# Kernel tuning notes

Hardware: AMD Instinct MI355X
Metric: run time of the kernel (lower is better)

Reference implementation:

```python
import jax, jax.numpy as jnp
import numpy as np

N_NODES = 50000
N_EDGES = 800000
SD = 128
N_GRAPHS = 128
HL = 4
VOCAB = 1340
N_CLASSES = 41
BN_EPS = 1e-5


def setup_inputs() -> dict:
    key = jax.random.key(0)
    ks = jax.random.split(key, 20)
    s = 1.0 / np.sqrt(SD)
    inp = {
        "node_ids": jax.random.randint(ks[0], (N_NODES,), 0, VOCAB),
        "edge_index": jax.random.randint(ks[1], (2, N_EDGES), 0, N_NODES),
        "batch": jnp.sort(jax.random.randint(ks[2], (N_NODES,), 0, N_GRAPHS)),
        "emb": jax.random.normal(ks[3], (VOCAB, SD)) * 0.05,
        "in_W1": jax.random.normal(ks[4], (SD, SD)) * s,
        "in_b1": jnp.zeros((SD,)),
        "in_W2": jax.random.normal(ks[5], (SD, SD)) * s,
        "in_b2": jnp.zeros((SD,)),
        "bn_gamma": jnp.ones((SD,)),
        "bn_beta": jnp.zeros((SD,)),
        "bn_mean": jnp.zeros((SD,)),
        "bn_var": jnp.ones((SD,)),
        "out_W1": jax.random.normal(ks[6], (SD, SD)) * s,
        "out_b1": jnp.zeros((SD,)),
        "out_W2": jax.random.normal(ks[7], (SD, SD)) * s,
        "out_b2": jnp.zeros((SD,)),
        "fc1_W": jax.random.normal(ks[8], (SD, SD)) * s,
        "fc1_b": jnp.zeros((SD,)),
        "fc2_W": jax.random.normal(ks[9], (N_CLASSES, SD)) * s,
        "fc2_b": jnp.zeros((N_CLASSES,)),
    }
    return inp


def reference(node_ids, edge_index, batch, emb, in_W1, in_b1, in_W2, in_b2,
              bn_gamma, bn_beta, bn_mean, bn_var,
              out_W1, out_b1, out_W2, out_b2, fc1_W, fc1_b, fc2_W, fc2_b):
    src, dst = edge_index[0], edge_index[1]

    def gin(x, W1, b1, W2, b2):
        # GINConv with eps=0: mlp(x + sum_{j in N(i)} x_j)
        agg = jax.ops.segment_sum(x[src], dst, num_segments=N_NODES)
        h = x + agg
        h = jnp.maximum(h @ W1.T + b1, 0.0)
        return h @ W2.T + b2

    def bn(x):
        # eval-mode BatchNorm1d with running stats
        return (x - bn_mean) * (bn_gamma / jnp.sqrt(bn_var + BN_EPS)) + bn_beta

    x = emb[node_ids]  # [N, SD]
    x = bn(jnp.maximum(gin(x, in_W1, in_b1, in_W2, in_b2), 0.0))
    for _ in range(HL):  # shared weights, repeated hl times
        x = bn(jnp.maximum(gin(x, in_W1, in_b1, in_W2, in_b2), 0.0))
    x = jnp.maximum(gin(x, out_W1, out_b1, out_W2, out_b2), 0.0)
    pooled = jax.ops.segment_sum(x, batch, num_segments=N_GRAPHS)  # [G, SD]
    h = jnp.maximum(pooled @ fc1_W.T + fc1_b, 0.0)
    return h @ fc2_W.T + fc2_b  # [G, 41]
```

## Files before the change

kernel.cpp:

```cpp
#include <hip/hip_runtime.h>

#define NN 50000
#define NE 800000
#define NG 128
#define NC 41
#define CAP 64

typedef __attribute__((ext_vector_type(8))) short bfrag8;
typedef __attribute__((ext_vector_type(4))) float facc4;

__device__ __forceinline__ float bf2f(unsigned short u) {
  union { unsigned int i; float f; } v; v.i = ((unsigned int)u) << 16; return v.f;
}
__device__ __forceinline__ unsigned short f2bf(float f) {
  union { float f; unsigned int i; } v; v.f = f;
  unsigned int x = v.i;
  x += 0x7fffu + ((x >> 16) & 1u);
  return (unsigned short)(x >> 16);
}
__device__ __forceinline__ void acc_u4(const uint4 u, float* a) {
  union { unsigned int i; float f; } c;
  c.i = u.x << 16;          a[0] += c.f;
  c.i = u.x & 0xffff0000u;  a[1] += c.f;
  c.i = u.y << 16;          a[2] += c.f;
  c.i = u.y & 0xffff0000u;  a[3] += c.f;
  c.i = u.z << 16;          a[4] += c.f;
  c.i = u.z & 0xffff0000u;  a[5] += c.f;
  c.i = u.w << 16;          a[6] += c.f;
  c.i = u.w & 0xffff0000u;  a[7] += c.f;
}
__device__ __forceinline__ unsigned int pack2(float lo, float hi) {
  return (unsigned int)f2bf(lo) | ((unsigned int)f2bf(hi) << 16);
}

__global__ void prep_kernel(const float* __restrict__ W1, const float* __restrict__ W2,
                            const float* __restrict__ oW1, const float* __restrict__ oW2,
                            const float* __restrict__ gamma, const float* __restrict__ beta,
                            const float* __restrict__ mean, const float* __restrict__ var,
                            unsigned short* W1b, unsigned short* W2b,
                            unsigned short* oW1b, unsigned short* oW2b,
                            float* scale, float* shift) {
  int i = blockIdx.x * 256 + threadIdx.x;
  if (i < 128 * 128) {
    W1b[i] = f2bf(W1[i]);
    W2b[i] = f2bf(W2[i]);
    oW1b[i] = f2bf(oW1[i]);
    oW2b[i] = f2bf(oW2[i]);
  }
  if (i < 128) {
    float s = gamma[i] * rsqrtf(var[i] + 1e-5f);
    scale[i] = s;
    shift[i] = beta[i] - mean[i] * s;
  }
}

__global__ void embed_kernel(const int* __restrict__ node_ids, const float* __restrict__ emb,
                             unsigned short* __restrict__ xb) {
  int idx = blockIdx.x * 256 + threadIdx.x;
  if (idx >= NN * 32) return;
  int node = idx >> 5, f = (idx & 31) * 4;
  const float4 v = *(const float4*)&emb[node_ids[node] * 128 + f];
  ushort4 o;
  o.x = f2bf(v.x); o.y = f2bf(v.y); o.z = f2bf(v.z); o.w = f2bf(v.w);
  *(ushort4*)&xb[node * 128 + f] = o;
}

__global__ void fill_kernel(const int* __restrict__ ei, int* __restrict__ cnt,
                            int* __restrict__ srclist) {
  int e = blockIdx.x * 256 + threadIdx.x;
  if (e >= NE) return;
  int s = ei[e];
  int d = ei[NE + e];
  int pos = atomicAdd(&cnt[d], 1);
  if (pos < CAP) srclist[d * CAP + pos] = s;
}

__global__ __launch_bounds__(256) void agg_kernel(const unsigned short* __restrict__ xb,
                                                  const int* __restrict__ cnt,
                                                  const int* __restrict__ srclist,
                                                  unsigned short* __restrict__ hb) {
  int tid = threadIdx.x;
  int node = blockIdx.x * 16 + (tid >> 4);
  if (node >= NN) return;
  int f = (tid & 15) * 8;
  float a[8];
  acc_u4(*(const uint4*)&xb[node * 128 + f],
         (a[0]=0.f, a[1]=0.f, a[2]=0.f, a[3]=0.f, a[4]=0.f, a[5]=0.f, a[6]=0.f, a[7]=0.f, a));
  int deg = cnt[node];
  if (deg > CAP) deg = CAP;
  const int* lst = &srclist[node * CAP];
  int j = 0;
  for (; j + 8 <= deg; j += 8) {
    uint4 u0 = *(const uint4*)&xb[lst[j] * 128 + f];
    uint4 u1 = *(const uint4*)&xb[lst[j + 1] * 128 + f];
    uint4 u2 = *(const uint4*)&xb[lst[j + 2] * 128 + f];
    uint4 u3 = *(const uint4*)&xb[lst[j + 3] * 128 + f];
    uint4 u4 = *(const uint4*)&xb[lst[j + 4] * 128 + f];
    uint4 u5 = *(const uint4*)&xb[lst[j + 5] * 128 + f];
    uint4 u6 = *(const uint4*)&xb[lst[j + 6] * 128 + f];
    uint4 u7 = *(const uint4*)&xb[lst[j + 7] * 128 + f];
    acc_u4(u0, a); acc_u4(u1, a); acc_u4(u2, a); acc_u4(u3, a);
    acc_u4(u4, a); acc_u4(u5, a); acc_u4(u6, a); acc_u4(u7, a);
  }
  for (; j + 4 <= deg; j += 4) {
    uint4 u0 = *(const uint4*)&xb[lst[j] * 128 + f];
    uint4 u1 = *(const uint4*)&xb[lst[j + 1] * 128 + f];
    uint4 u2 = *(const uint4*)&xb[lst[j + 2] * 128 + f];
    uint4 u3 = *(const uint4*)&xb[lst[j + 3] * 128 + f];
    acc_u4(u0, a); acc_u4(u1, a); acc_u4(u2, a); acc_u4(u3, a);
  }
  for (; j < deg; ++j) {
    uint4 u = *(const uint4*)&xb[lst[j] * 128 + f];
    acc_u4(u, a);
  }
  uint4 o;
  o.x = pack2(a[0], a[1]); o.y = pack2(a[2], a[3]);
  o.z = pack2(a[4], a[5]); o.w = pack2(a[6], a[7]);
  *(uint4*)&hb[node * 128 + f] = o;
}

__global__ __launch_bounds__(512) void mlp_kernel(const unsigned short* __restrict__ A,
                                                  const unsigned short* __restrict__ W1b,
                                                  const unsigned short* __restrict__ W2b,
                                                  const float* __restrict__ bias1,
                                                  const float* __restrict__ bias2,
                                                  const float* __restrict__ scale,
                                                  const float* __restrict__ shift,
                                                  unsigned short* __restrict__ Out,
                                                  int M, int mode) {
  __shared__ unsigned short sW1[128][136];
  __shared__ unsigned short sW2[128][136];
  __shared__ unsigned short sA[128][136];
  __shared__ unsigned short sT[128][136];
  int tid = threadIdx.x;
  int bRow = blockIdx.x * 128;

  const uint4* gw1 = (const uint4*)W1b;
  const uint4* gw2 = (const uint4*)W2b;
#pragma unroll
  for (int p = 0; p < 4; ++p) {
    int idx = (p * 512 + tid) * 8;
    int r = idx >> 7, c = idx & 127;
    *(uint4*)&sW1[r][c] = gw1[p * 512 + tid];
    *(uint4*)&sW2[r][c] = gw2[p * 512 + tid];
  }
#pragma unroll
  for (int p = 0; p < 4; ++p) {
    int idx = (p * 512 + tid) * 8;
    int r = idx >> 7, c = idx & 127;
    int grow = bRow + r;
    uint4 v = {0u, 0u, 0u, 0u};
    if (grow < M) v = *(const uint4*)&A[grow * 128 + c];
    *(uint4*)&sA[r][c] = v;
  }
  __syncthreads();

  int wave = tid >> 6;
  int lane = tid & 63;
  int l16 = lane & 15;
  int quad = lane >> 4;
  int arow = wave * 16 + l16;

  {
    facc4 acc[8];
#pragma unroll
    for (int t = 0; t < 8; ++t) acc[t] = (facc4){0.f, 0.f, 0.f, 0.f};
#pragma unroll
    for (int k = 0; k < 4; ++k) {
      bfrag8 af = *(const bfrag8*)&sA[arow][k * 32 + quad * 8];
#pragma unroll
      for (int t = 0; t < 8; ++t) {
        bfrag8 bf = *(const bfrag8*)&sW1[t * 16 + l16][k * 32 + quad * 8];
        acc[t] = __builtin_amdgcn_mfma_f32_16x16x32_bf16(af, bf, acc[t], 0, 0, 0);
      }
    }
#pragma unroll
    for (int t = 0; t < 8; ++t) {
      int col = t * 16 + l16;
      float b = bias1[col];
#pragma unroll
      for (int i = 0; i < 4; ++i) {
        int row = wave * 16 + quad * 4 + i;
        float v = acc[t][i] + b;
        sT[row][col] = f2bf(v > 0.f ? v : 0.f);
      }
    }
  }
  __syncthreads();

  {
    facc4 acc[8];
#pragma unroll
    for (int t = 0; t < 8; ++t) acc[t] = (facc4){0.f, 0.f, 0.f, 0.f};
#pragma unroll
    for (int k = 0; k < 4; ++k) {
      bfrag8 af = *(const bfrag8*)&sT[arow][k * 32 + quad * 8];
#pragma unroll
      for (int t = 0; t < 8; ++t) {
        bfrag8 bf = *(const bfrag8*)&sW2[t * 16 + l16][k * 32 + quad * 8];
        acc[t] = __builtin_amdgcn_mfma_f32_16x16x32_bf16(af, bf, acc[t], 0, 0, 0);
      }
    }
#pragma unroll
    for (int t = 0; t < 8; ++t) {
      int col = t * 16 + l16;
      float b = bias2[col];
      float sc = 1.f, sh = 0.f;
      if (mode == 1) { sc = scale[col]; sh = shift[col]; }
#pragma unroll
      for (int i = 0; i < 4; ++i) {
        int row = wave * 16 + quad * 4 + i;
        float v = acc[t][i] + b;
        v = v > 0.f ? v : 0.f;
        if (mode == 1) v = v * sc + sh;
        sA[row][col] = f2bf(v);
      }
    }
  }
  __syncthreads();

#pragma unroll
  for (int p = 0; p < 4; ++p) {
    int idx = (p * 512 + tid) * 8;
    int r = idx >> 7, c = idx & 127;
    int grow = bRow + r;
    if (grow < M) *(uint4*)&Out[grow * 128 + c] = *(const uint4*)&sA[r][c];
  }
}

__global__ __launch_bounds__(128) void pool_kernel(const unsigned short* __restrict__ xb,
                                                   const int* __restrict__ batch,
                                                   float* __restrict__ pooled) {
  const int CHUNK = 128;
  int start = blockIdx.x * CHUNK;
  int end = start + CHUNK;
  if (end > NN) end = NN;
  int f = threadIdx.x;
  float acc = 0.f;
  int cur = -1;
  for (int i = start; i < end; ++i) {
    int b = batch[i];
    if (b != cur) {
      if (cur >= 0) atomicAdd(&pooled[cur * 128 + f], acc);
      cur = b;
      acc = 0.f;
    }
    acc += bf2f(xb[i * 128 + f]);
  }
  if (cur >= 0) atomicAdd(&pooled[cur * 128 + f], acc);
}

__global__ void fc1_kernel(const float* __restrict__ pooled, const float* __restrict__ W,
                           const float* __restrict__ b, float* __restrict__ out) {
  int idx = blockIdx.x * 256 + threadIdx.x;
  if (idx >= NG * 128) return;
  int r = idx >> 7, c = idx & 127;
  float acc = 0.f;
  for (int k = 0; k < 128; ++k) acc += pooled[r * 128 + k] * W[c * 128 + k];
  acc += b[c];
  out[idx] = acc > 0.f ? acc : 0.f;
}

__global__ void fc2_kernel(const float* __restrict__ h1, const float* __restrict__ W,
                           const float* __restrict__ b, float* __restrict__ out) {
  int idx = blockIdx.x * 256 + threadIdx.x;
  if (idx >= NG * NC) return;
  int r = idx / NC, c = idx % NC;
  float acc = 0.f;
  for (int k = 0; k < 128; ++k) acc += h1[r * 128 + k] * W[c * 128 + k];
  out[idx] = acc + b[c];
}

extern "C" void kernel_launch(void* const* d_in, const int* in_sizes, int n_in,
                              void* d_out, int out_size, void* d_ws, size_t ws_size,
                              hipStream_t stream) {
  const int* node_ids = (const int*)d_in[0];
  const int* edge_index = (const int*)d_in[1];
  const int* batch = (const int*)d_in[2];
  const float* emb = (const float*)d_in[3];
  const float* in_W1 = (const float*)d_in[4];
  const float* in_b1 = (const float*)d_in[5];
  const float* in_W2 = (const float*)d_in[6];
  const float* in_b2 = (const float*)d_in[7];
  const float* bn_gamma = (const float*)d_in[8];
  const float* bn_beta = (const float*)d_in[9];
  const float* bn_mean = (const float*)d_in[10];
  const float* bn_var = (const float*)d_in[11];
  const float* out_W1 = (const float*)d_in[12];
  const float* out_b1 = (const float*)d_in[13];
  const float* out_W2 = (const float*)d_in[14];
  const float* out_b2 = (const float*)d_in[15];
  const float* fc1_W = (const float*)d_in[16];
  const float* fc1_b = (const float*)d_in[17];
  const float* fc2_W = (const float*)d_in[18];
  const float* fc2_b = (const float*)d_in[19];
  float* out = (float*)d_out;

  char* ws = (char*)d_ws;
  size_t off = 0;
  auto alloc = [&](size_t bytes) {
    char* p = ws + off;
    off = (off + bytes + 255) & ~(size_t)255;
    return p;
  };
  unsigned short* xb = (unsigned short*)alloc((size_t)NN * 128 * 2);
  unsigned short* hb = (unsigned short*)alloc((size_t)NN * 128 * 2);
  int* srclist = (int*)alloc((size_t)NN * CAP * 4);
  int* cnt = (int*)alloc((size_t)NN * 4);
  unsigned short* W1b = (unsigned short*)alloc(128 * 128 * 2);
  unsigned short* W2b = (unsigned short*)alloc(128 * 128 * 2);
  unsigned short* oW1b = (unsigned short*)alloc(128 * 128 * 2);
  unsigned short* oW2b = (unsigned short*)alloc(128 * 128 * 2);
  float* bnscale = (float*)alloc(128 * 4);
  float* bnshift = (float*)alloc(128 * 4);
  float* pooled = (float*)alloc(NG * 128 * 4);
  float* h1 = (float*)alloc(NG * 128 * 4);

  hipMemsetAsync(cnt, 0, (size_t)NN * 4, stream);
  hipMemsetAsync(pooled, 0, (size_t)NG * 128 * 4, stream);

  prep_kernel<<<64, 256, 0, stream>>>(in_W1, in_W2, out_W1, out_W2,
                                      bn_gamma, bn_beta, bn_mean, bn_var,
                                      W1b, W2b, oW1b, oW2b, bnscale, bnshift);
  fill_kernel<<<(NE + 255) / 256, 256, 0, stream>>>(edge_index, cnt, srclist);
  embed_kernel<<<(NN * 32 + 255) / 256, 256, 0, stream>>>(node_ids, emb, xb);

  int mlp_blocks = (NN + 127) / 128;
  for (int l = 0; l < 6; ++l) {
    const unsigned short* w1 = (l < 5) ? W1b : oW1b;
    const unsigned short* w2 = (l < 5) ? W2b : oW2b;
    const float* b1 = (l < 5) ? in_b1 : out_b1;
    const float* b2 = (l < 5) ? in_b2 : out_b2;
    int mode2 = (l < 5) ? 1 : 0;
    agg_kernel<<<(NN + 15) / 16, 256, 0, stream>>>(xb, cnt, srclist, hb);
    mlp_kernel<<<mlp_blocks, 512, 0, stream>>>(hb, w1, w2, b1, b2, bnscale, bnshift,
                                               xb, NN, mode2);
  }

  pool_kernel<<<(NN + 127) / 128, 128, 0, stream>>>(xb, batch, pooled);
  fc1_kernel<<<(NG * 128 + 255) / 256, 256, 0, stream>>>(pooled, fc1_W, fc1_b, h1);
  fc2_kernel<<<(NG * NC + 255) / 256, 256, 0, stream>>>(h1, fc2_W, fc2_b, out);
}
```

Measured before the change: 497.8 us.

## Shrink MLP tile to 64 rows, swizzle LDS, reuse A buffer in place

The fused two-layer MLP kernel now processes 64 rows per 256-thread block instead of 128 rows per 512 threads. The padded shared arrays are replaced by an XOR-free rotation swizzle, and the intermediate buffer sT is dropped: A fragments are loaded into registers first and the hidden activations are written back into sA. The intermediate __syncthreads is also removed, relying on each wave touching only its own 16 rows. This cuts LDS use for occupancy, but every block reloads both weight matrices, so weight staging traffic doubles.

```diff
diff --git a/kernel.cpp b/kernel.cpp
--- a/kernel.cpp
+++ b/kernel.cpp
@@ -119,7 +119,7 @@
   *(uint4*)&hb[node * 128 + f] = o;
 }
 
-__global__ __launch_bounds__(512) void mlp_kernel(const unsigned short* __restrict__ A,
+__global__ __launch_bounds__(256) void mlp_kernel(const unsigned short* __restrict__ A,
                                                   const unsigned short* __restrict__ W1b,
                                                   const unsigned short* __restrict__ W2b,
                                                   const float* __restrict__ bias1,
@@ -128,30 +128,31 @@
                                                   const float* __restrict__ shift,
                                                   unsigned short* __restrict__ Out,
                                                   int M, int mode) {
-  __shared__ unsigned short sW1[128][136];
-  __shared__ unsigned short sW2[128][136];
-  __shared__ unsigned short sA[128][136];
-  __shared__ unsigned short sT[128][136];
+  __shared__ unsigned short sW1[128 * 128];
+  __shared__ unsigned short sW2[128 * 128];
+  __shared__ unsigned short sA[64 * 128];
   int tid = threadIdx.x;
-  int bRow = blockIdx.x * 128;
+  int bRow = blockIdx.x * 64;
 
   const uint4* gw1 = (const uint4*)W1b;
   const uint4* gw2 = (const uint4*)W2b;
 #pragma unroll
+  for (int p = 0; p < 8; ++p) {
+    int g = p * 256 + tid;
+    int r = g >> 4, b = g & 15;
+    int ph = (b + r) & 15;
+    *(uint4*)&sW1[(r * 16 + ph) * 8] = gw1[g];
+    *(uint4*)&sW2[(r * 16 + ph) * 8] = gw2[g];
+  }
+#pragma unroll
   for (int p = 0; p < 4; ++p) {
-    int idx = (p * 512 + tid) * 8;
-    int r = idx >> 7, c = idx & 127;
-    *(uint4*)&sW1[r][c] = gw1[p * 512 + tid];
-    *(uint4*)&sW2[r][c] = gw2[p * 512 + tid];
-  }
-#pragma unroll
-  for (int p = 0; p < 4; ++p) {
-    int idx = (p * 512 + tid) * 8;
-    int r = idx >> 7, c = idx & 127;
+    int g = p * 256 + tid;
+    int r = g >> 4, b = g & 15;
+    int ph = (b + r) & 15;
     int grow = bRow + r;
     uint4 v = {0u, 0u, 0u, 0u};
-    if (grow < M) v = *(const uint4*)&A[grow * 128 + c];
-    *(uint4*)&sA[r][c] = v;
+    if (grow < M) v = *(const uint4*)&A[grow * 128 + b * 8];
+    *(uint4*)&sA[(r * 16 + ph) * 8] = v;
   }
   __syncthreads();
 
@@ -162,43 +163,58 @@
   int arow = wave * 16 + l16;
 
   {
+    bfrag8 af[4];
+#pragma unroll
+    for (int k = 0; k < 4; ++k) {
+      int ph = (k * 4 + quad + arow) & 15;
+      af[k] = *(const bfrag8*)&sA[(arow * 16 + ph) * 8];
+    }
     facc4 acc[8];
 #pragma unroll
     for (int t = 0; t < 8; ++t) acc[t] = (facc4){0.f, 0.f, 0.f, 0.f};
 #pragma unroll
     for (int k = 0; k < 4; ++k) {
-      bfrag8 af = *(const bfrag8*)&sA[arow][k * 32 + quad * 8];
 #pragma unroll
       for (int t = 0; t < 8; ++t) {
-        bfrag8 bf = *(const bfrag8*)&sW1[t * 16 + l16][k * 32 + quad * 8];
-        acc[t] = __builtin_amdgcn_mfma_f32_16x16x32_bf16(af, bf, acc[t], 0, 0, 0);
+        int r = t * 16 + l16;
+        int ph = (k * 4 + quad + r) & 15;
+        bfrag8 bf = *(const bfrag8*)&sW1[(r * 16 + ph) * 8];
+        acc[t] = __builtin_amdgcn_mfma_f32_16x16x32_bf16(af[k], bf, acc[t], 0, 0, 0);
       }
     }
 #pragma unroll
     for (int t = 0; t < 8; ++t) {
       int col = t * 16 + l16;
       float b = bias1[col];
+      int cb = col >> 3, ce = col & 7;
 #pragma unroll
       for (int i = 0; i < 4; ++i) {
         int row = wave * 16 + quad * 4 + i;
         float v = acc[t][i] + b;
-        sT[row][col] = f2bf(v > 0.f ? v : 0.f);
+        int ph = (cb + row) & 15;
+        sA[(row * 16 + ph) * 8 + ce] = f2bf(v > 0.f ? v : 0.f);
       }
     }
   }
-  __syncthreads();
 
   {
+    bfrag8 af[4];
+#pragma unroll
+    for (int k = 0; k < 4; ++k) {
+      int ph = (k * 4 + quad + arow) & 15;
+      af[k] = *(const bfrag8*)&sA[(arow * 16 + ph) * 8];
+    }
     facc4 acc[8];
 #pragma unroll
     for (int t = 0; t < 8; ++t) acc[t] = (facc4){0.f, 0.f, 0.f, 0.f};
 #pragma unroll
     for (int k = 0; k < 4; ++k) {
-      bfrag8 af = *(const bfrag8*)&sT[arow][k * 32 + quad * 8];
 #pragma unroll
       for (int t = 0; t < 8; ++t) {
-        bfrag8 bf = *(const bfrag8*)&sW2[t * 16 + l16][k * 32 + quad * 8];
-        acc[t] = __builtin_amdgcn_mfma_f32_16x16x32_bf16(af, bf, acc[t], 0, 0, 0);
+        int r = t * 16 + l16;
+        int ph = (k * 4 + quad + r) & 15;
+        bfrag8 bf = *(const bfrag8*)&sW2[(r * 16 + ph) * 8];
+        acc[t] = __builtin_amdgcn_mfma_f32_16x16x32_bf16(af[k], bf, acc[t], 0, 0, 0);
       }
     }
 #pragma unroll
@@ -207,13 +223,15 @@
       float b = bias2[col];
       float sc = 1.f, sh = 0.f;
       if (mode == 1) { sc = scale[col]; sh = shift[col]; }
+      int cb = col >> 3, ce = col & 7;
 #pragma unroll
       for (int i = 0; i < 4; ++i) {
         int row = wave * 16 + quad * 4 + i;
         float v = acc[t][i] + b;
         v = v > 0.f ? v : 0.f;
         if (mode == 1) v = v * sc + sh;
-        sA[row][col] = f2bf(v);
+        int ph = (cb + row) & 15;
+        sA[(row * 16 + ph) * 8 + ce] = f2bf(v);
       }
     }
   }
@@ -221,10 +239,12 @@
 
 #pragma unroll
   for (int p = 0; p < 4; ++p) {
-    int idx = (p * 512 + tid) * 8;
-    int r = idx >> 7, c = idx & 127;
+    int g = p * 256 + tid;
+    int r = g >> 4, b = g & 15;
+    int ph = (b + r) & 15;
     int grow = bRow + r;
-    if (grow < M) *(uint4*)&Out[grow * 128 + c] = *(const uint4*)&sA[r][c];
+    if (grow < M)
+      *(uint4*)&Out[grow * 128 + b * 8] = *(const uint4*)&sA[(r * 16 + ph) * 8];
   }
 }
 
@@ -325,7 +345,7 @@
   fill_kernel<<<(NE + 255) / 256, 256, 0, stream>>>(edge_index, cnt, srclist);
   embed_kernel<<<(NN * 32 + 255) / 256, 256, 0, stream>>>(node_ids, emb, xb);
 
-  int mlp_blocks = (NN + 127) / 128;
+  int mlp_blocks = (NN + 63) / 64;
   for (int l = 0; l < 6; ++l) {
     const unsigned short* w1 = (l < 5) ? W1b : oW1b;
     const unsigned short* w2 = (l < 5) ? W2b : oW2b;
@@ -333,7 +353,7 @@
     const float* b2 = (l < 5) ? in_b2 : out_b2;
     int mode2 = (l < 5) ? 1 : 0;
     agg_kernel<<<(NN + 15) / 16, 256, 0, stream>>>(xb, cnt, srclist, hb);
-    mlp_kernel<<<mlp_blocks, 512, 0, stream>>>(hb, w1, w2, b1, b2, bnscale, bnshift,
+    mlp_kernel<<<mlp_blocks, 256, 0, stream>>>(hb, w1, w2, b1, b2, bnscale, bnshift,
                                                xb, NN, mode2);
   }
 
```

New measurement: 502.7 us. Within noise of the previous version (+1.0%).
